# Kernel tuning notes

Measured on AMD Instinct MI355X. Metric: run time of the kernel, lower is better.

## Reference

```python
import jax, jax.numpy as jnp
import numpy as np

U, P, D, H, E = 512, 1024, 128, 256, 98304
N = U + P


def setup_inputs() -> dict:
    key = jax.random.key(0)
    ks = jax.random.split(key, 16)
    def nrm(k, shape, scale=0.05):
        return jax.random.normal(k, shape, jnp.float32) * scale
    z = lambda *s: jnp.zeros(s, jnp.float32)
    return {
        "user_ids": jnp.arange(U),
        "paper_ids": jnp.arange(P),
        "edge_index": jax.random.randint(ks[0], (2, E), 0, N),
        "user_paper_interactions": jax.random.uniform(ks[1], (U, P), jnp.float32),
        "user_emb": nrm(ks[2], (U, D), 1.0),   # nn.Embedding tables
        "paper_emb": nrm(ks[3], (P, D), 1.0),
        "W0": nrm(ks[4], (D, H)), "b0": z(H),   # GCNConv weights (stored [in,out])
        "W1": nrm(ks[5], (H, H)), "b1": z(H),
        "W2": nrm(ks[6], (H, H)), "b2": z(H),
        "Wu": nrm(ks[7], (H, D)), "bu": z(D),   # user_output Linear
        "Wp": nrm(ks[8], (H, D)), "bp": z(D),   # paper_output Linear
        "Wq1": nrm(ks[9], (2 * D, H)), "bq1": z(H),  # predictor Linear 1
        "Wq2": nrm(ks[10], (H, 1)), "bq2": z(1),      # predictor Linear 2
    }


def gcn_conv(x, src, dst, W, b):
    """PyG GCNConv: add self-loops, symmetric D^-1/2 (A+I) D^-1/2 normalization."""
    n = x.shape[0]
    loop = jnp.arange(n)
    s = jnp.concatenate([src, loop])
    d = jnp.concatenate([dst, loop])
    deg = jax.ops.segment_sum(jnp.ones(d.shape, x.dtype), d, num_segments=n)
    dis = jnp.where(deg > 0, jax.lax.rsqrt(jnp.maximum(deg, 1.0)), 0.0)
    norm = dis[s] * dis[d]                      # [E+n]
    h = x @ W                                   # [n, H]
    out = jax.ops.segment_sum(h[s] * norm[:, None], d, num_segments=n)
    return out + b


def reference(user_ids, paper_ids, edge_index, user_paper_interactions,
              user_emb, paper_emb, W0, b0, W1, b1, W2, b2,
              Wu, bu, Wp, bp, Wq1, bq1, Wq2, bq2):
    # embedding lookups + node feature matrix [U+P, D]
    x = jnp.concatenate([user_emb[user_ids], paper_emb[paper_ids]], axis=0)
    src, dst = edge_index[0], edge_index[1]
    for W, b in ((W0, b0), (W1, b1), (W2, b2)):
        x = jax.nn.relu(gcn_conv(x, src, dst, W, b))  # dropout is identity in eval
    nu = user_ids.shape[0]
    np_ = paper_ids.shape[0]
    user_final = x[:nu] @ Wu + bu               # [U, D]
    paper_final = x[nu:] @ Wp + bp              # [P, D]
    # broadcast outer-product concat -> [U, P, 2D]
    combined = jnp.concatenate([
        jnp.broadcast_to(user_final[:, None, :], (nu, np_, user_final.shape[-1])),
        jnp.broadcast_to(paper_final[None, :, :], (nu, np_, paper_final.shape[-1])),
    ], axis=-1)
    h = jax.nn.relu(combined @ Wq1 + bq1)       # [U, P, H]
    pred = jax.nn.sigmoid(h @ Wq2 + bq2)[..., 0]  # [U, P]
    return pred
```

## Files before the change

### kernel.cpp

```cpp
#include <hip/hip_runtime.h>
#include <math.h>

constexpr int Uc = 512;
constexpr int Pc = 1024;
constexpr int Dc = 128;
constexpr int Hc = 256;
constexpr int Ec = 98304;
constexpr int Nc = 1536;
constexpr int CAP = 192;

__device__ __forceinline__ void fma4(float4& a, float n, const float4 r) {
    a.x += n * r.x; a.y += n * r.y; a.z += n * r.z; a.w += n * r.w;
}

template <int K>
__device__ __forceinline__ void gemm_core16(const float* __restrict__ xr,
                                            const float* __restrict__ wc, int M,
                                            float& acc0, float& acc1) {
#pragma unroll 4
    for (int k = 0; k < K; k += 4) {
        float4 a = *(const float4*)(xr + k);
        float2 b0 = *(const float2*)(wc + (size_t)k * M);
        float2 b1 = *(const float2*)(wc + (size_t)(k + 1) * M);
        float2 b2 = *(const float2*)(wc + (size_t)(k + 2) * M);
        float2 b3 = *(const float2*)(wc + (size_t)(k + 3) * M);
        acc0 += a.x * b0.x; acc1 += a.x * b0.y;
        acc0 += a.y * b1.x; acc1 += a.y * b1.y;
        acc0 += a.z * b2.x; acc1 += a.z * b2.y;
        acc0 += a.w * b3.x; acc1 += a.w * b3.y;
    }
}

__global__ void k_front(const int* __restrict__ e_src, const int* __restrict__ e_dst,
                        int* __restrict__ cnt, int* __restrict__ colF,
                        const float* __restrict__ Wu, const float* __restrict__ Wp,
                        const float* __restrict__ Wq1, const float* __restrict__ bu,
                        const float* __restrict__ bp, const float* __restrict__ bq1,
                        float* __restrict__ Wup, float* __restrict__ Wpp,
                        float* __restrict__ bvu, float* __restrict__ bvp) {
    int t = threadIdx.x, b = blockIdx.x;
    if (b < 384) {
        int e = b * 256 + t;
        int d = e_dst[e];
        int pos = atomicAdd(&cnt[d], 1);
        if (pos < CAP) colF[d * CAP + pos] = e_src[e];
    } else if (b < 640) {
        int id = b - 384;
        int z = id >> 7, tile = id & 127;
        int tx = t & 15, ty = t >> 4;
        const float* X = z ? Wp : Wu;
        const float* W = Wq1 + (z ? (size_t)Dc * Hc : 0);
        float* Y = z ? Wpp : Wup;
        int row = (tile >> 3) * 16 + ty, col = (tile & 7) * 32 + tx * 2;
        float a0 = 0.f, a1 = 0.f;
        gemm_core16<Dc>(X + (size_t)row * Dc, W + col, Hc, a0, a1);
        *(float2*)&Y[(size_t)row * Hc + col] = make_float2(a0, a1);
    } else if (b == 640) {
        float s = bq1[t];
#pragma unroll 8
        for (int d = 0; d < Dc; d++) s += bu[d] * Wq1[d * Hc + t];
        bvu[t] = s;
    } else {
        float s = 0.f;
#pragma unroll 8
        for (int d = 0; d < Dc; d++) s += bp[d] * Wq1[(Dc + d) * Hc + t];
        bvp[t] = s;
    }
}

__global__ void k_l0(const int* __restrict__ uid, const int* __restrict__ pid,
                     const float* __restrict__ ue, const float* __restrict__ pe,
                     const float* __restrict__ W0, const float* __restrict__ b0,
                     const int* __restrict__ cnt, const int* __restrict__ colF,
                     float* __restrict__ out) {
    __shared__ const float* sptr[2][CAP];
    __shared__ float snrm[2][CAP];
    __shared__ __align__(16) float pagg[4][Dc];
    __shared__ __align__(16) float agg[2][Dc];
    int t = threadIdx.x, b = blockIdx.x;
    int ibase = b * 2;
    int c[2]; float di[2];
#pragma unroll
    for (int r = 0; r < 2; r++) {
        c[r] = cnt[ibase + r];
        di[r] = rsqrtf((float)(c[r] + 1));
        int deg = min(c[r], CAP);
        if (t < deg) {
            int s = colF[(ibase + r) * CAP + t];
            sptr[r][t] = (s < Uc) ? ue + (size_t)uid[s] * Dc
                                  : pe + (size_t)pid[s - Uc] * Dc;
            snrm[r][t] = rsqrtf((float)(cnt[s] + 1));
        }
    }
    __syncthreads();
    {
        int wv = t >> 6, ln = t & 63;
        int r = wv >> 1, h = wv & 1;
        int i = ibase + r;
        int dg = min(c[r], CAP);
        int dg2 = dg >> 1;
        int j0 = h ? dg2 : 0, j1 = h ? dg : dg2;
        float2 acc = make_float2(0.f, 0.f);
        if (h == 0) {
            const float* xi = (i < Uc) ? ue + (size_t)uid[i] * Dc
                                       : pe + (size_t)pid[i - Uc] * Dc;
            float2 a2 = *(const float2*)(xi + ln * 2);
            acc.x = di[r] * a2.x;
            acc.y = di[r] * a2.y;
        }
        int j = j0;
        for (; j + 4 <= j1; j += 4) {
            float n0 = snrm[r][j],     n1 = snrm[r][j + 1];
            float n2 = snrm[r][j + 2], n3 = snrm[r][j + 3];
            float2 r0 = *(const float2*)(sptr[r][j] + ln * 2);
            float2 r1 = *(const float2*)(sptr[r][j + 1] + ln * 2);
            float2 r2 = *(const float2*)(sptr[r][j + 2] + ln * 2);
            float2 r3 = *(const float2*)(sptr[r][j + 3] + ln * 2);
            acc.x += n0 * r0.x + n1 * r1.x + n2 * r2.x + n3 * r3.x;
            acc.y += n0 * r0.y + n1 * r1.y + n2 * r2.y + n3 * r3.y;
        }
        for (; j < j1; j++) {
            float2 r0 = *(const float2*)(sptr[r][j] + ln * 2);
            acc.x += snrm[r][j] * r0.x;
            acc.y += snrm[r][j] * r0.y;
        }
        pagg[wv][ln * 2]     = acc.x;
        pagg[wv][ln * 2 + 1] = acc.y;
    }
    __syncthreads();
    {
        int r = t >> 7, f = t & 127;
        agg[r][f] = di[r] * (pagg[2 * r][f] + pagg[2 * r + 1][f]);
    }
    __syncthreads();
    float a0 = 0.f, a1 = 0.f;
#pragma unroll 2
    for (int k = 0; k < Dc; k += 4) {
        float4 g0 = *(const float4*)&agg[0][k];
        float4 g1 = *(const float4*)&agg[1][k];
        float w0 = W0[(size_t)(k + 0) * Hc + t];
        float w1 = W0[(size_t)(k + 1) * Hc + t];
        float w2 = W0[(size_t)(k + 2) * Hc + t];
        float w3 = W0[(size_t)(k + 3) * Hc + t];
        a0 += g0.x * w0 + g0.y * w1 + g0.z * w2 + g0.w * w3;
        a1 += g1.x * w0 + g1.y * w1 + g1.z * w2 + g1.w * w3;
    }
    float bb = b0[t];
    out[(size_t)(ibase + 0) * Hc + t] = fmaxf(a0 + bb, 0.f);
    out[(size_t)(ibase + 1) * Hc + t] = fmaxf(a1 + bb, 0.f);
}

__device__ __forceinline__ void agg_wave2(const float* __restrict__ X,
                                          const int (*sidx)[CAP], const float (*snrm)[CAP],
                                          const int* c, const float* di, int ibase,
                                          float (*pagg)[Hc], int t) {
    int wv = t >> 6, ln = t & 63;
    int r = wv >> 1, h = wv & 1;
    int dg = min(c[r], CAP);
    int dg2 = dg >> 1;
    int j0 = h ? dg2 : 0, j1 = h ? dg : dg2;
    float4 acc = make_float4(0.f, 0.f, 0.f, 0.f);
    if (h == 0) {
        acc = *(const float4*)&X[(size_t)(ibase + r) * Hc + ln * 4];
        acc.x *= di[r]; acc.y *= di[r]; acc.z *= di[r]; acc.w *= di[r];
    }
    int j = j0;
    for (; j + 4 <= j1; j += 4) {
        float n0 = snrm[r][j],     n1 = snrm[r][j + 1];
        float n2 = snrm[r][j + 2], n3 = snrm[r][j + 3];
        float4 r0 = *(const float4*)&X[sidx[r][j]     + ln * 4];
        float4 r1 = *(const float4*)&X[sidx[r][j + 1] + ln * 4];
        float4 r2 = *(const float4*)&X[sidx[r][j + 2] + ln * 4];
        float4 r3 = *(const float4*)&X[sidx[r][j + 3] + ln * 4];
        fma4(acc, n0, r0); fma4(acc, n1, r1); fma4(acc, n2, r2); fma4(acc, n3, r3);
    }
    for (; j < j1; j++) {
        float4 r0 = *(const float4*)&X[sidx[r][j] + ln * 4];
        fma4(acc, snrm[r][j], r0);
    }
    *(float4*)&pagg[wv][ln * 4] = acc;
}

__global__ void k_lh(const float* __restrict__ X, const float* __restrict__ W,
                     const float* __restrict__ bias, const int* __restrict__ cnt,
                     const int* __restrict__ colF, float* __restrict__ out) {
    __shared__ int sidx[2][CAP];
    __shared__ float snrm[2][CAP];
    __shared__ __align__(16) float pagg[4][Hc];
    __shared__ __align__(16) float agg[2][Hc];
    int t = threadIdx.x, b = blockIdx.x;
    int ibase = b * 2;
    int c[2]; float di[2];
#pragma unroll
    for (int r = 0; r < 2; r++) {
        c[r] = cnt[ibase + r];
        di[r] = rsqrtf((float)(c[r] + 1));
        int deg = min(c[r], CAP);
        if (t < deg) {
            int s = colF[(ibase + r) * CAP + t];
            sidx[r][t] = s * Hc;
            snrm[r][t] = rsqrtf((float)(cnt[s] + 1));
        }
    }
    __syncthreads();
    agg_wave2(X, sidx, snrm, c, di, ibase, pagg, t);
    __syncthreads();
    agg[0][t] = di[0] * (pagg[0][t] + pagg[1][t]);
    agg[1][t] = di[1] * (pagg[2][t] + pagg[3][t]);
    __syncthreads();
    float a0 = 0.f, a1 = 0.f;
#pragma unroll 2
    for (int k = 0; k < Hc; k += 4) {
        float4 g0 = *(const float4*)&agg[0][k];
        float4 g1 = *(const float4*)&agg[1][k];
        float w0 = W[(size_t)(k + 0) * Hc + t];
        float w1 = W[(size_t)(k + 1) * Hc + t];
        float w2 = W[(size_t)(k + 2) * Hc + t];
        float w3 = W[(size_t)(k + 3) * Hc + t];
        a0 += g0.x * w0 + g0.y * w1 + g0.z * w2 + g0.w * w3;
        a1 += g1.x * w0 + g1.y * w1 + g1.z * w2 + g1.w * w3;
    }
    float bb = bias[t];
    out[(size_t)(ibase + 0) * Hc + t] = fmaxf(a0 + bb, 0.f);
    out[(size_t)(ibase + 1) * Hc + t] = fmaxf(a1 + bb, 0.f);
}

__global__ void k_lht(const float* __restrict__ X, const float* __restrict__ W2,
                      const float* __restrict__ b2, const int* __restrict__ cnt,
                      const int* __restrict__ colF,
                      const float* __restrict__ Wup, const float* __restrict__ Wpp,
                      const float* __restrict__ bvu, const float* __restrict__ bvp,
                      float* __restrict__ AuT, float* __restrict__ ApT) {
    __shared__ int sidx[2][CAP];
    __shared__ float snrm[2][CAP];
    __shared__ __align__(16) float pagg[4][Hc];
    __shared__ __align__(16) float agg[2][Hc];
    __shared__ __align__(16) float xloc[2][Hc];
    int t = threadIdx.x, b = blockIdx.x;
    int ibase = b * 2;
    int c[2]; float di[2];
#pragma unroll
    for (int r = 0; r < 2; r++) {
        c[r] = cnt[ibase + r];
        di[r] = rsqrtf((float)(c[r] + 1));
        int deg = min(c[r], CAP);
        if (t < deg) {
            int s = colF[(ibase + r) * CAP + t];
            sidx[r][t] = s * Hc;
            snrm[r][t] = rsqrtf((float)(cnt[s] + 1));
        }
    }
    __syncthreads();
    agg_wave2(X, sidx, snrm, c, di, ibase, pagg, t);
    __syncthreads();
    agg[0][t] = di[0] * (pagg[0][t] + pagg[1][t]);
    agg[1][t] = di[1] * (pagg[2][t] + pagg[3][t]);
    __syncthreads();
    {
        float a0 = 0.f, a1 = 0.f;
#pragma unroll 2
        for (int k = 0; k < Hc; k += 4) {
            float4 g0 = *(const float4*)&agg[0][k];
            float4 g1 = *(const float4*)&agg[1][k];
            float w0 = W2[(size_t)(k + 0) * Hc + t];
            float w1 = W2[(size_t)(k + 1) * Hc + t];
            float w2 = W2[(size_t)(k + 2) * Hc + t];
            float w3 = W2[(size_t)(k + 3) * Hc + t];
            a0 += g0.x * w0 + g0.y * w1 + g0.z * w2 + g0.w * w3;
            a1 += g1.x * w0 + g1.y * w1 + g1.z * w2 + g1.w * w3;
        }
        float bb = b2[t];
        xloc[0][t] = fmaxf(a0 + bb, 0.f);
        xloc[1][t] = fmaxf(a1 + bb, 0.f);
    }
    __syncthreads();
    {
        const float* Wsel = (b < 256) ? Wup : Wpp;
        const float* bsel = (b < 256) ? bvu : bvp;
        float* YT  = (b < 256) ? AuT : ApT;
        int ldy    = (b < 256) ? Uc : Pc;
        int rloc   = (b < 256) ? ibase : ibase - Uc;
        float a0 = 0.f, a1 = 0.f;
#pragma unroll 2
        for (int k = 0; k < Hc; k += 4) {
            float4 g0 = *(const float4*)&xloc[0][k];
            float4 g1 = *(const float4*)&xloc[1][k];
            float w0 = Wsel[(size_t)(k + 0) * Hc + t];
            float w1 = Wsel[(size_t)(k + 1) * Hc + t];
            float w2 = Wsel[(size_t)(k + 2) * Hc + t];
            float w3 = Wsel[(size_t)(k + 3) * Hc + t];
            a0 += g0.x * w0 + g0.y * w1 + g0.z * w2 + g0.w * w3;
            a1 += g1.x * w0 + g1.y * w1 + g1.z * w2 + g1.w * w3;
        }
        float bb = bsel[t];
        *(float2*)&YT[(size_t)t * ldy + rloc] = make_float2(a0 + bb, a1 + bb);
    }
}

__global__ void k_pred(const float* __restrict__ AuT, const float* __restrict__ ApT,
                       const float* __restrict__ Wq2, const float* __restrict__ bq2,
                       float* __restrict__ out) {
    __shared__ float auS[Hc * 16];
    int t = threadIdx.x;
    int ub = blockIdx.x * 16, pb = blockIdx.y * 64;
#pragma unroll
    for (int i = t; i < Hc * 16; i += 256) {
        int k = i >> 4, u = i & 15;
        auS[i] = AuT[(size_t)k * Uc + ub + u];
    }
    __syncthreads();
    int uu = t >> 5;
    int pp = t & 31;
    const float* app = ApT + pb + pp * 2;
    const float* aup = auS + uu * 2;
    float acc[2][2] = {};
#pragma unroll 4
    for (int k = 0; k < Hc; k += 4) {
        float4 wv = *(const float4*)&Wq2[k];
        float2 a[4], p2[4];
#pragma unroll
        for (int j = 0; j < 4; j++) a[j] = *(const float2*)(aup + (k + j) * 16);
#pragma unroll
        for (int j = 0; j < 4; j++) p2[j] = *(const float2*)(app + (size_t)(k + j) * Pc);
        const float* w = (const float*)&wv;
#pragma unroll
        for (int j = 0; j < 4; j++) {
            float a0 = a[j].x, a1 = a[j].y;
            float p0 = p2[j].x, p1 = p2[j].y;
            acc[0][0] += fmaxf(a0 + p0, 0.f) * w[j];
            acc[0][1] += fmaxf(a0 + p1, 0.f) * w[j];
            acc[1][0] += fmaxf(a1 + p0, 0.f) * w[j];
            acc[1][1] += fmaxf(a1 + p1, 0.f) * w[j];
        }
    }
    float bq = bq2[0];
#pragma unroll
    for (int r = 0; r < 2; r++) {
        int u = ub + uu * 2 + r;
        float2 o;
        o.x = 1.f / (1.f + __expf(-(acc[r][0] + bq)));
        o.y = 1.f / (1.f + __expf(-(acc[r][1] + bq)));
        *(float2*)&out[(size_t)u * Pc + pb + pp * 2] = o;
    }
}


extern "C" void kernel_launch(void* const* d_in, const int* in_sizes, int n_in,
                              void* d_out, int out_size, void* d_ws, size_t ws_size,
                              hipStream_t stream) {
    const int*   uid = (const int*)d_in[0];
    const int*   pid = (const int*)d_in[1];
    const int*   ei  = (const int*)d_in[2];
    const float* ue  = (const float*)d_in[4];
    const float* pe  = (const float*)d_in[5];
    const float* W0  = (const float*)d_in[6];  const float* b0 = (const float*)d_in[7];
    const float* W1  = (const float*)d_in[8];  const float* b1 = (const float*)d_in[9];
    const float* W2  = (const float*)d_in[10]; const float* b2 = (const float*)d_in[11];
    const float* Wu  = (const float*)d_in[12]; const float* bu = (const float*)d_in[13];
    const float* Wp  = (const float*)d_in[14]; const float* bp = (const float*)d_in[15];
    const float* Wq1 = (const float*)d_in[16]; const float* bq1 = (const float*)d_in[17];
    const float* Wq2 = (const float*)d_in[18]; const float* bq2 = (const float*)d_in[19];

    const int* e_src = ei;
    const int* e_dst = ei + Ec;

    char* w = (char*)d_ws;
    auto alloc = [&](size_t bytes) { char* p = w; w += (bytes + 255) & ~size_t(255); return p; };
    int*   cnt  = (int*)alloc(Nc * 4);
    int*   colF = (int*)alloc((size_t)Nc * CAP * 4);
    float* xA   = (float*)alloc((size_t)Nc * Hc * 4);
    float* xB   = (float*)alloc((size_t)Nc * Hc * 4);
    float* Wup  = (float*)alloc((size_t)Hc * Hc * 4);
    float* Wpp  = (float*)alloc((size_t)Hc * Hc * 4);
    float* bvu  = (float*)alloc(Hc * 4);
    float* bvp  = (float*)alloc(Hc * 4);
    float* AuT  = (float*)alloc((size_t)Hc * Uc * 4);
    float* ApT  = (float*)alloc((size_t)Hc * Pc * 4);
    float* pred = (float*)d_out;

    hipMemsetAsync(cnt, 0, Nc * 4, stream);
    k_front<<<642, 256, 0, stream>>>(e_src, e_dst, cnt, colF, Wu, Wp, Wq1,
                                     bu, bp, bq1, Wup, Wpp, bvu, bvp);
    k_l0<<<Nc / 2, 256, 0, stream>>>(uid, pid, ue, pe, W0, b0, cnt, colF, xA);
    k_lh<<<Nc / 2, 256, 0, stream>>>(xA, W1, b1, cnt, colF, xB);
    k_lht<<<Nc / 2, 256, 0, stream>>>(xB, W2, b2, cnt, colF, Wup, Wpp, bvu, bvp, AuT, ApT);
    k_pred<<<dim3(Uc / 16, Pc / 64), 256, 0, stream>>>(AuT, ApT, Wq2, bq2, pred);
}
```

Measured before the change: 195.5 us.

## Split GEMV over K across waves, unroll gathers by 8, retile predictor

The per-node GEMVs in the three GCN layer kernels now split the K dimension across the four waves. Each lane computes four output columns with float4 weight loads, and the partial sums are reduced through shared memory. The neighbour-gather loops get an extra 8-way unrolled path to keep more loads in flight, and launch bounds are added. The pairwise predictor kernel is retiled to 8 users by 256 papers per block with float4 paper loads and a 2x4 register tile. The cost is extra shared memory and one more barrier for the reduction.

```diff
diff --git a/kernel.cpp b/kernel.cpp
--- a/kernel.cpp
+++ b/kernel.cpp
@@ -68,15 +68,17 @@
     }
 }
 
-__global__ void k_l0(const int* __restrict__ uid, const int* __restrict__ pid,
-                     const float* __restrict__ ue, const float* __restrict__ pe,
-                     const float* __restrict__ W0, const float* __restrict__ b0,
-                     const int* __restrict__ cnt, const int* __restrict__ colF,
-                     float* __restrict__ out) {
+__global__ void __launch_bounds__(256) k_l0(
+        const int* __restrict__ uid, const int* __restrict__ pid,
+        const float* __restrict__ ue, const float* __restrict__ pe,
+        const float* __restrict__ W0, const float* __restrict__ b0,
+        const int* __restrict__ cnt, const int* __restrict__ colF,
+        float* __restrict__ out) {
     __shared__ const float* sptr[2][CAP];
     __shared__ float snrm[2][CAP];
     __shared__ __align__(16) float pagg[4][Dc];
-    __shared__ __align__(16) float agg[2][Dc];
+    __shared__ __align__(16) float aggT[Dc][2];
+    __shared__ __align__(16) float red[4][2][Hc];
     int t = threadIdx.x, b = blockIdx.x;
     int ibase = b * 2;
     int c[2]; float di[2];
@@ -109,10 +111,28 @@
             acc.y = di[r] * a2.y;
         }
         int j = j0;
+        for (; j + 8 <= j1; j += 8) {
+            float n0 = snrm[r][j],     n1 = snrm[r][j + 1];
+            float n2 = snrm[r][j + 2], n3 = snrm[r][j + 3];
+            float n4 = snrm[r][j + 4], n5 = snrm[r][j + 5];
+            float n6 = snrm[r][j + 6], n7 = snrm[r][j + 7];
+            float2 r0 = *(const float2*)(sptr[r][j]     + ln * 2);
+            float2 r1 = *(const float2*)(sptr[r][j + 1] + ln * 2);
+            float2 r2 = *(const float2*)(sptr[r][j + 2] + ln * 2);
+            float2 r3 = *(const float2*)(sptr[r][j + 3] + ln * 2);
+            float2 r4 = *(const float2*)(sptr[r][j + 4] + ln * 2);
+            float2 r5 = *(const float2*)(sptr[r][j + 5] + ln * 2);
+            float2 r6 = *(const float2*)(sptr[r][j + 6] + ln * 2);
+            float2 r7 = *(const float2*)(sptr[r][j + 7] + ln * 2);
+            acc.x += n0 * r0.x + n1 * r1.x + n2 * r2.x + n3 * r3.x;
+            acc.y += n0 * r0.y + n1 * r1.y + n2 * r2.y + n3 * r3.y;
+            acc.x += n4 * r4.x + n5 * r5.x + n6 * r6.x + n7 * r7.x;
+            acc.y += n4 * r4.y + n5 * r5.y + n6 * r6.y + n7 * r7.y;
+        }
         for (; j + 4 <= j1; j += 4) {
             float n0 = snrm[r][j],     n1 = snrm[r][j + 1];
             float n2 = snrm[r][j + 2], n3 = snrm[r][j + 3];
-            float2 r0 = *(const float2*)(sptr[r][j] + ln * 2);
+            float2 r0 = *(const float2*)(sptr[r][j]     + ln * 2);
             float2 r1 = *(const float2*)(sptr[r][j + 1] + ln * 2);
             float2 r2 = *(const float2*)(sptr[r][j + 2] + ln * 2);
             float2 r3 = *(const float2*)(sptr[r][j + 3] + ln * 2);
@@ -130,24 +150,32 @@
     __syncthreads();
     {
         int r = t >> 7, f = t & 127;
-        agg[r][f] = di[r] * (pagg[2 * r][f] + pagg[2 * r + 1][f]);
-    }
-    __syncthreads();
-    float a0 = 0.f, a1 = 0.f;
-#pragma unroll 2
-    for (int k = 0; k < Dc; k += 4) {
-        float4 g0 = *(const float4*)&agg[0][k];
-        float4 g1 = *(const float4*)&agg[1][k];
-        float w0 = W0[(size_t)(k + 0) * Hc + t];
-        float w1 = W0[(size_t)(k + 1) * Hc + t];
-        float w2 = W0[(size_t)(k + 2) * Hc + t];
-        float w3 = W0[(size_t)(k + 3) * Hc + t];
-        a0 += g0.x * w0 + g0.y * w1 + g0.z * w2 + g0.w * w3;
-        a1 += g1.x * w0 + g1.y * w1 + g1.z * w2 + g1.w * w3;
-    }
-    float bb = b0[t];
-    out[(size_t)(ibase + 0) * Hc + t] = fmaxf(a0 + bb, 0.f);
-    out[(size_t)(ibase + 1) * Hc + t] = fmaxf(a1 + bb, 0.f);
+        aggT[f][r] = di[r] * (pagg[2 * r][f] + pagg[2 * r + 1][f]);
+    }
+    __syncthreads();
+    {
+        int wv = t >> 6, ln = t & 63;
+        int k0 = wv * (Dc / 4);
+        float4 a0 = {0.f, 0.f, 0.f, 0.f}, a1 = {0.f, 0.f, 0.f, 0.f};
+        const float* Wp_ = W0 + (size_t)k0 * Hc + ln * 4;
+#pragma unroll 8
+        for (int kk = 0; kk < Dc / 4; kk++) {
+            float2 g = *(const float2*)&aggT[k0 + kk][0];
+            float4 w = *(const float4*)(Wp_ + (size_t)kk * Hc);
+            a0.x += g.x * w.x; a0.y += g.x * w.y; a0.z += g.x * w.z; a0.w += g.x * w.w;
+            a1.x += g.y * w.x; a1.y += g.y * w.y; a1.z += g.y * w.z; a1.w += g.y * w.w;
+        }
+        *(float4*)&red[wv][0][ln * 4] = a0;
+        *(float4*)&red[wv][1][ln * 4] = a1;
+    }
+    __syncthreads();
+    {
+        float bb = b0[t];
+        float s0 = (red[0][0][t] + red[1][0][t]) + (red[2][0][t] + red[3][0][t]) + bb;
+        float s1 = (red[0][1][t] + red[1][1][t]) + (red[2][1][t] + red[3][1][t]) + bb;
+        out[(size_t)(ibase + 0) * Hc + t] = fmaxf(s0, 0.f);
+        out[(size_t)(ibase + 1) * Hc + t] = fmaxf(s1, 0.f);
+    }
 }
 
 __device__ __forceinline__ void agg_wave2(const float* __restrict__ X,
@@ -165,6 +193,22 @@
         acc.x *= di[r]; acc.y *= di[r]; acc.z *= di[r]; acc.w *= di[r];
     }
     int j = j0;
+    for (; j + 8 <= j1; j += 8) {
+        float n0 = snrm[r][j],     n1 = snrm[r][j + 1];
+        float n2 = snrm[r][j + 2], n3 = snrm[r][j + 3];
+        float n4 = snrm[r][j + 4], n5 = snrm[r][j + 5];
+        float n6 = snrm[r][j + 6], n7 = snrm[r][j + 7];
+        float4 r0 = *(const float4*)&X[sidx[r][j]     + ln * 4];
+        float4 r1 = *(const float4*)&X[sidx[r][j + 1] + ln * 4];
+        float4 r2 = *(const float4*)&X[sidx[r][j + 2] + ln * 4];
+        float4 r3 = *(const float4*)&X[sidx[r][j + 3] + ln * 4];
+        float4 r4 = *(const float4*)&X[sidx[r][j + 4] + ln * 4];
+        float4 r5 = *(const float4*)&X[sidx[r][j + 5] + ln * 4];
+        float4 r6 = *(const float4*)&X[sidx[r][j + 6] + ln * 4];
+        float4 r7 = *(const float4*)&X[sidx[r][j + 7] + ln * 4];
+        fma4(acc, n0, r0); fma4(acc, n1, r1); fma4(acc, n2, r2); fma4(acc, n3, r3);
+        fma4(acc, n4, r4); fma4(acc, n5, r5); fma4(acc, n6, r6); fma4(acc, n7, r7);
+    }
     for (; j + 4 <= j1; j += 4) {
         float n0 = snrm[r][j],     n1 = snrm[r][j + 1];
         float n2 = snrm[r][j + 2], n3 = snrm[r][j + 3];
@@ -181,13 +225,33 @@
     *(float4*)&pagg[wv][ln * 4] = acc;
 }
 
-__global__ void k_lh(const float* __restrict__ X, const float* __restrict__ W,
-                     const float* __restrict__ bias, const int* __restrict__ cnt,
-                     const int* __restrict__ colF, float* __restrict__ out) {
+__device__ __forceinline__ void gemv_wsplit(const float (*aggT)[2],
+                                            const float* __restrict__ W,
+                                            float (*red)[2][Hc], int t) {
+    int wv = t >> 6, ln = t & 63;
+    int k0 = wv * (Hc / 4);
+    float4 a0 = {0.f, 0.f, 0.f, 0.f}, a1 = {0.f, 0.f, 0.f, 0.f};
+    const float* Wp_ = W + (size_t)k0 * Hc + ln * 4;
+#pragma unroll 8
+    for (int kk = 0; kk < Hc / 4; kk++) {
+        float2 g = *(const float2*)&aggT[k0 + kk][0];
+        float4 w = *(const float4*)(Wp_ + (size_t)kk * Hc);
+        a0.x += g.x * w.x; a0.y += g.x * w.y; a0.z += g.x * w.z; a0.w += g.x * w.w;
+        a1.x += g.y * w.x; a1.y += g.y * w.y; a1.z += g.y * w.z; a1.w += g.y * w.w;
+    }
+    *(float4*)&red[wv][0][ln * 4] = a0;
+    *(float4*)&red[wv][1][ln * 4] = a1;
+}
+
+__global__ void __launch_bounds__(256) k_lh(
+        const float* __restrict__ X, const float* __restrict__ W,
+        const float* __restrict__ bias, const int* __restrict__ cnt,
+        const int* __restrict__ colF, float* __restrict__ out) {
     __shared__ int sidx[2][CAP];
     __shared__ float snrm[2][CAP];
     __shared__ __align__(16) float pagg[4][Hc];
-    __shared__ __align__(16) float agg[2][Hc];
+    __shared__ __align__(16) float aggT[Hc][2];
+    __shared__ __align__(16) float red[4][2][Hc];
     int t = threadIdx.x, b = blockIdx.x;
     int ibase = b * 2;
     int c[2]; float di[2];
@@ -205,37 +269,33 @@
     __syncthreads();
     agg_wave2(X, sidx, snrm, c, di, ibase, pagg, t);
     __syncthreads();
-    agg[0][t] = di[0] * (pagg[0][t] + pagg[1][t]);
-    agg[1][t] = di[1] * (pagg[2][t] + pagg[3][t]);
-    __syncthreads();
-    float a0 = 0.f, a1 = 0.f;
-#pragma unroll 2
-    for (int k = 0; k < Hc; k += 4) {
-        float4 g0 = *(const float4*)&agg[0][k];
-        float4 g1 = *(const float4*)&agg[1][k];
-        float w0 = W[(size_t)(k + 0) * Hc + t];
-        float w1 = W[(size_t)(k + 1) * Hc + t];
-        float w2 = W[(size_t)(k + 2) * Hc + t];
-        float w3 = W[(size_t)(k + 3) * Hc + t];
-        a0 += g0.x * w0 + g0.y * w1 + g0.z * w2 + g0.w * w3;
-        a1 += g1.x * w0 + g1.y * w1 + g1.z * w2 + g1.w * w3;
-    }
-    float bb = bias[t];
-    out[(size_t)(ibase + 0) * Hc + t] = fmaxf(a0 + bb, 0.f);
-    out[(size_t)(ibase + 1) * Hc + t] = fmaxf(a1 + bb, 0.f);
-}
-
-__global__ void k_lht(const float* __restrict__ X, const float* __restrict__ W2,
-                      const float* __restrict__ b2, const int* __restrict__ cnt,
-                      const int* __restrict__ colF,
-                      const float* __restrict__ Wup, const float* __restrict__ Wpp,
-                      const float* __restrict__ bvu, const float* __restrict__ bvp,
-                      float* __restrict__ AuT, float* __restrict__ ApT) {
+    *(float2*)&aggT[t][0] = make_float2(di[0] * (pagg[0][t] + pagg[1][t]),
+                                        di[1] * (pagg[2][t] + pagg[3][t]));
+    __syncthreads();
+    gemv_wsplit(aggT, W, red, t);
+    __syncthreads();
+    {
+        float bb = bias[t];
+        float s0 = (red[0][0][t] + red[1][0][t]) + (red[2][0][t] + red[3][0][t]) + bb;
+        float s1 = (red[0][1][t] + red[1][1][t]) + (red[2][1][t] + red[3][1][t]) + bb;
+        out[(size_t)(ibase + 0) * Hc + t] = fmaxf(s0, 0.f);
+        out[(size_t)(ibase + 1) * Hc + t] = fmaxf(s1, 0.f);
+    }
+}
+
+__global__ void __launch_bounds__(256) k_lht(
+        const float* __restrict__ X, const float* __restrict__ W2,
+        const float* __restrict__ b2, const int* __restrict__ cnt,
+        const int* __restrict__ colF,
+        const float* __restrict__ Wup, const float* __restrict__ Wpp,
+        const float* __restrict__ bvu, const float* __restrict__ bvp,
+        float* __restrict__ AuT, float* __restrict__ ApT) {
     __shared__ int sidx[2][CAP];
     __shared__ float snrm[2][CAP];
     __shared__ __align__(16) float pagg[4][Hc];
-    __shared__ __align__(16) float agg[2][Hc];
-    __shared__ __align__(16) float xloc[2][Hc];
+    __shared__ __align__(16) float aggT[Hc][2];
+    __shared__ __align__(16) float xlocT[Hc][2];
+    __shared__ __align__(16) float red[4][2][Hc];
     int t = threadIdx.x, b = blockIdx.x;
     int ibase = b * 2;
     int c[2]; float di[2];
@@ -253,94 +313,76 @@
     __syncthreads();
     agg_wave2(X, sidx, snrm, c, di, ibase, pagg, t);
     __syncthreads();
-    agg[0][t] = di[0] * (pagg[0][t] + pagg[1][t]);
-    agg[1][t] = di[1] * (pagg[2][t] + pagg[3][t]);
-    __syncthreads();
-    {
-        float a0 = 0.f, a1 = 0.f;
-#pragma unroll 2
-        for (int k = 0; k < Hc; k += 4) {
-            float4 g0 = *(const float4*)&agg[0][k];
-            float4 g1 = *(const float4*)&agg[1][k];
-            float w0 = W2[(size_t)(k + 0) * Hc + t];
-            float w1 = W2[(size_t)(k + 1) * Hc + t];
-            float w2 = W2[(size_t)(k + 2) * Hc + t];
-            float w3 = W2[(size_t)(k + 3) * Hc + t];
-            a0 += g0.x * w0 + g0.y * w1 + g0.z * w2 + g0.w * w3;
-            a1 += g1.x * w0 + g1.y * w1 + g1.z * w2 + g1.w * w3;
-        }
+    *(float2*)&aggT[t][0] = make_float2(di[0] * (pagg[0][t] + pagg[1][t]),
+                                        di[1] * (pagg[2][t] + pagg[3][t]));
+    __syncthreads();
+    gemv_wsplit(aggT, W2, red, t);
+    __syncthreads();
+    {
         float bb = b2[t];
-        xloc[0][t] = fmaxf(a0 + bb, 0.f);
-        xloc[1][t] = fmaxf(a1 + bb, 0.f);
+        float s0 = (red[0][0][t] + red[1][0][t]) + (red[2][0][t] + red[3][0][t]) + bb;
+        float s1 = (red[0][1][t] + red[1][1][t]) + (red[2][1][t] + red[3][1][t]) + bb;
+        *(float2*)&xlocT[t][0] = make_float2(fmaxf(s0, 0.f), fmaxf(s1, 0.f));
     }
     __syncthreads();
     {
         const float* Wsel = (b < 256) ? Wup : Wpp;
+        gemv_wsplit(xlocT, Wsel, red, t);
+    }
+    __syncthreads();
+    {
         const float* bsel = (b < 256) ? bvu : bvp;
         float* YT  = (b < 256) ? AuT : ApT;
         int ldy    = (b < 256) ? Uc : Pc;
         int rloc   = (b < 256) ? ibase : ibase - Uc;
-        float a0 = 0.f, a1 = 0.f;
-#pragma unroll 2
-        for (int k = 0; k < Hc; k += 4) {
-            float4 g0 = *(const float4*)&xloc[0][k];
-            float4 g1 = *(const float4*)&xloc[1][k];
-            float w0 = Wsel[(size_t)(k + 0) * Hc + t];
-            float w1 = Wsel[(size_t)(k + 1) * Hc + t];
-            float w2 = Wsel[(size_t)(k + 2) * Hc + t];
-            float w3 = Wsel[(size_t)(k + 3) * Hc + t];
-            a0 += g0.x * w0 + g0.y * w1 + g0.z * w2 + g0.w * w3;
-            a1 += g1.x * w0 + g1.y * w1 + g1.z * w2 + g1.w * w3;
-        }
         float bb = bsel[t];
-        *(float2*)&YT[(size_t)t * ldy + rloc] = make_float2(a0 + bb, a1 + bb);
-    }
-}
-
-__global__ void k_pred(const float* __restrict__ AuT, const float* __restrict__ ApT,
-                       const float* __restrict__ Wq2, const float* __restrict__ bq2,
-                       float* __restrict__ out) {
-    __shared__ float auS[Hc * 16];
+        float s0 = (red[0][0][t] + red[1][0][t]) + (red[2][0][t] + red[3][0][t]) + bb;
+        float s1 = (red[0][1][t] + red[1][1][t]) + (red[2][1][t] + red[3][1][t]) + bb;
+        *(float2*)&YT[(size_t)t * ldy + rloc] = make_float2(s0, s1);
+    }
+}
+
+__global__ void __launch_bounds__(256) k_pred(
+        const float* __restrict__ AuT, const float* __restrict__ ApT,
+        const float* __restrict__ Wq2, const float* __restrict__ bq2,
+        float* __restrict__ out) {
+    __shared__ float auS[Hc * 8];
     int t = threadIdx.x;
-    int ub = blockIdx.x * 16, pb = blockIdx.y * 64;
+    int ub = blockIdx.x * 8, pb = blockIdx.y * 256;
 #pragma unroll
-    for (int i = t; i < Hc * 16; i += 256) {
-        int k = i >> 4, u = i & 15;
+    for (int i = t; i < Hc * 8; i += 256) {
+        int k = i >> 3, u = i & 7;
         auS[i] = AuT[(size_t)k * Uc + ub + u];
     }
     __syncthreads();
-    int uu = t >> 5;
-    int pp = t & 31;
-    const float* app = ApT + pb + pp * 2;
-    const float* aup = auS + uu * 2;
-    float acc[2][2] = {};
+    int wv = t >> 6, ln = t & 63;
+    const float* app = ApT + pb + ln * 4;
+    const float* aup = auS + wv * 2;
+    float acc[2][4] = {};
 #pragma unroll 4
-    for (int k = 0; k < Hc; k += 4) {
-        float4 wv = *(const float4*)&Wq2[k];
-        float2 a[4], p2[4];
-#pragma unroll
-        for (int j = 0; j < 4; j++) a[j] = *(const float2*)(aup + (k + j) * 16);
-#pragma unroll
-        for (int j = 0; j < 4; j++) p2[j] = *(const float2*)(app + (size_t)(k + j) * Pc);
-        const float* w = (const float*)&wv;
-#pragma unroll
-        for (int j = 0; j < 4; j++) {
-            float a0 = a[j].x, a1 = a[j].y;
-            float p0 = p2[j].x, p1 = p2[j].y;
-            acc[0][0] += fmaxf(a0 + p0, 0.f) * w[j];
-            acc[0][1] += fmaxf(a0 + p1, 0.f) * w[j];
-            acc[1][0] += fmaxf(a1 + p0, 0.f) * w[j];
-            acc[1][1] += fmaxf(a1 + p1, 0.f) * w[j];
-        }
+    for (int k = 0; k < Hc; k++) {
+        float w = Wq2[k];
+        float2 a = *(const float2*)(aup + k * 8);
+        float4 p = *(const float4*)(app + (size_t)k * Pc);
+        acc[0][0] += fmaxf(a.x + p.x, 0.f) * w;
+        acc[0][1] += fmaxf(a.x + p.y, 0.f) * w;
+        acc[0][2] += fmaxf(a.x + p.z, 0.f) * w;
+        acc[0][3] += fmaxf(a.x + p.w, 0.f) * w;
+        acc[1][0] += fmaxf(a.y + p.x, 0.f) * w;
+        acc[1][1] += fmaxf(a.y + p.y, 0.f) * w;
+        acc[1][2] += fmaxf(a.y + p.z, 0.f) * w;
+        acc[1][3] += fmaxf(a.y + p.w, 0.f) * w;
     }
     float bq = bq2[0];
 #pragma unroll
     for (int r = 0; r < 2; r++) {
-        int u = ub + uu * 2 + r;
-        float2 o;
+        int u = ub + wv * 2 + r;
+        float4 o;
         o.x = 1.f / (1.f + __expf(-(acc[r][0] + bq)));
         o.y = 1.f / (1.f + __expf(-(acc[r][1] + bq)));
-        *(float2*)&out[(size_t)u * Pc + pb + pp * 2] = o;
+        o.z = 1.f / (1.f + __expf(-(acc[r][2] + bq)));
+        o.w = 1.f / (1.f + __expf(-(acc[r][3] + bq)));
+        *(float4*)&out[(size_t)u * Pc + pb + ln * 4] = o;
     }
 }
 
@@ -384,5 +426,5 @@
     k_l0<<<Nc / 2, 256, 0, stream>>>(uid, pid, ue, pe, W0, b0, cnt, colF, xA);
     k_lh<<<Nc / 2, 256, 0, stream>>>(xA, W1, b1, cnt, colF, xB);
     k_lht<<<Nc / 2, 256, 0, stream>>>(xB, W2, b2, cnt, colF, Wup, Wpp, bvu, bvp, AuT, ApT);
-    k_pred<<<dim3(Uc / 16, Pc / 64), 256, 0, stream>>>(AuT, ApT, Wq2, bq2, pred);
-}
+    k_pred<<<dim3(Uc / 8, Pc / 256), 256, 0, stream>>>(AuT, ApT, Wq2, bq2, pred);
+}
```

After: 192.6 us. No clear change (-1.4%).
